# Kernel optimization log

Measured on AMD Instinct MI355X. Metric: run time of the kernel, lower is better.

The kernel has to match this reference:

```python
import jax, jax.numpy as jnp
import numpy as np

N_NODES = 50000
N_EDGES = 800000
IN_DIM = 100
OUT_DIM = 40
K_HOPS = 3


def setup_inputs() -> dict:
    key = jax.random.key(0)
    k1, k2, k3, k4 = jax.random.split(key, 4)
    feat = jax.random.normal(k1, (N_NODES, IN_DIM), dtype=jnp.float32)
    # fc params (PyTorch Linear default init scale ~ 1/sqrt(in_dim))
    W = jax.random.normal(k2, (OUT_DIM, IN_DIM), dtype=jnp.float32) / np.sqrt(IN_DIM)
    b = jnp.zeros((OUT_DIM,), dtype=jnp.float32)
    src = jax.random.randint(k3, (N_EDGES,), 0, N_NODES, dtype=jnp.int32)
    dst = jax.random.randint(k4, (N_EDGES,), 0, N_NODES, dtype=jnp.int32)
    return {"feat": feat, "W": W, "b": b, "src": src, "dst": dst}


def reference(feat, W, b, src, dst):
    n = feat.shape[0]
    # symmetric degree norm (DGL SGConv uses in-degrees, clamp(min=1))
    deg = jax.ops.segment_sum(jnp.ones_like(dst, dtype=feat.dtype), dst, num_segments=n)
    norm = jnp.maximum(deg, 1.0)[:, None] ** -0.5  # [N,1]
    h = feat
    for _ in range(K_HOPS):
        h = h * norm
        # SpMM: sum over incoming edges (gather src rows, scatter-add to dst)
        h = jax.ops.segment_sum(h[src], dst, num_segments=n)
        h = h * norm
    # user-supplied normalize: per-feature zero mean / unit std (unbiased std)
    h = (h - h.mean(axis=0)) / h.std(axis=0, ddof=1)
    # final linear classifier
    return h @ W.T + b
```

## Files before the change

kernel.cpp:

```cpp
#include <hip/hip_runtime.h>

#define N_NODES 50000
#define N_EDGES 800000
#define IN_DIM 100
#define OUT_DIM 40
#define ROW 50
#define ROW_PAD 64
#define SCAN_B 512
#define NSCAN_BLK ((N_NODES + SCAN_B - 1) / SCAN_B)
#define CSR_CAP (N_EDGES + N_NODES * 8 + 64)

typedef unsigned int uint;

__device__ __forceinline__ float bflo(uint u) { return __uint_as_float(u << 16); }
__device__ __forceinline__ float bfhi(uint u) { return __uint_as_float(u & 0xffff0000u); }
__device__ __forceinline__ uint packbf(float a, float b) {
    uint ua = __float_as_uint(a), ub = __float_as_uint(b);
    ua = (ua + 0x7fffu + ((ua >> 16) & 1u)) >> 16;
    ub = (ub + 0x7fffu + ((ub >> 16) & 1u)) >> 16;
    return ua | (ub << 16);
}

__global__ void zero_kernel(int* p, int n, uint* fs, uint* bufA, uint* bufB) {
    int i = blockIdx.x * blockDim.x + threadIdx.x;
    if (i < n) p[i] = 0;
    if (i < ROW_PAD) {
        fs[(size_t)N_NODES * ROW_PAD + i] = 0u;
        bufA[(size_t)N_NODES * ROW_PAD + i] = 0u;
        bufB[(size_t)N_NODES * ROW_PAD + i] = 0u;
    }
}

__global__ void deg_kernel(const int* __restrict__ dst, int* __restrict__ deg,
                           int* __restrict__ eoff) {
    int e = blockIdx.x * blockDim.x + threadIdx.x;
    if (e < N_EDGES) eoff[e] = atomicAdd(&deg[dst[e]], 1);
}

__global__ __launch_bounds__(SCAN_B) void scan1_kernel(const int* __restrict__ deg,
                                                       int* __restrict__ rowptr,
                                                       float* __restrict__ norm,
                                                       float* __restrict__ norm2,
                                                       int* __restrict__ blocksum) {
    int i = blockIdx.x * SCAN_B + threadIdx.x;
    int lane = threadIdx.x & 63, wid = threadIdx.x >> 6;
    int d = (i < N_NODES) ? deg[i] : 0;
    int da = (d + 7) & ~7;
    int v = da;
#pragma unroll
    for (int off = 1; off < 64; off <<= 1) {
        int t = __shfl_up(v, off);
        if (lane >= off) v += t;
    }
    __shared__ int wsum[8];
    if (lane == 63) wsum[wid] = v;
    __syncthreads();
    if (threadIdx.x < 8) {
        int w = wsum[threadIdx.x];
#pragma unroll
        for (int off = 1; off < 8; off <<= 1) {
            int t = __shfl_up(w, off);
            if (lane >= off) w += t;
        }
        wsum[threadIdx.x] = w;
    }
    __syncthreads();
    int woff = wid ? wsum[wid - 1] : 0;
    int incl = woff + v;
    if (i < N_NODES) {
        rowptr[i] = incl - da;
        float n1 = 1.0f / sqrtf((float)max(d, 1));
        norm[i] = n1;
        norm2[i] = n1 * n1;
    }
    if (threadIdx.x == SCAN_B - 1) blocksum[blockIdx.x] = incl;
}

__global__ __launch_bounds__(128) void scan2_kernel(const int* __restrict__ blocksum,
                                                    int* __restrict__ blockoff,
                                                    int* __restrict__ rowptr) {
    __shared__ int s[128];
    int t = threadIdx.x;
    int v = (t < NSCAN_BLK) ? blocksum[t] : 0;
    s[t] = v;
    __syncthreads();
    for (int off = 1; off < 128; off <<= 1) {
        int u = (t >= off) ? s[t - off] : 0;
        __syncthreads();
        s[t] += u;
        __syncthreads();
    }
    if (t < NSCAN_BLK) blockoff[t] = s[t] - v;
    if (t == 127) rowptr[N_NODES] = s[127];
}

__global__ __launch_bounds__(SCAN_B) void scan3_kernel(int* __restrict__ rowptr,
                                                       const int* __restrict__ blockoff,
                                                       const int* __restrict__ deg,
                                                       int* __restrict__ csr) {
    int i = blockIdx.x * SCAN_B + threadIdx.x;
    if (i < N_NODES) {
        int rp = rowptr[i] + blockoff[blockIdx.x];
        rowptr[i] = rp;
        int d = deg[i], da = (d + 7) & ~7;
        for (int k = d; k < da; ++k) csr[rp + k] = N_NODES;
    }
}

__global__ void csr_fill_kernel(const int* __restrict__ src, const int* __restrict__ dst,
                                const int* __restrict__ rowptr,
                                const int* __restrict__ eoff,
                                int* __restrict__ csr) {
    int e = blockIdx.x * blockDim.x + threadIdx.x;
    if (e < N_EDGES) csr[rowptr[dst[e]] + eoff[e]] = src[e];
}

__global__ __launch_bounds__(256) void prescale_kernel(const float* __restrict__ feat,
                                                       const float* __restrict__ norm,
                                                       uint4* __restrict__ fs4) {
    int t = blockIdx.x * 256 + threadIdx.x;
    if (t >= N_NODES * 16) return;
    int n = t >> 4, ql = t & 15;
    float nm = norm[n];
    uint4 o = make_uint4(0u, 0u, 0u, 0u);
    const float4* fr = (const float4*)(feat + (size_t)n * IN_DIM);
    if (ql < 12) {
        float4 a = fr[2 * ql], b2 = fr[2 * ql + 1];
        o.x = packbf(a.x * nm, a.y * nm);  o.y = packbf(a.z * nm, a.w * nm);
        o.z = packbf(b2.x * nm, b2.y * nm); o.w = packbf(b2.z * nm, b2.w * nm);
    } else if (ql == 12) {
        float4 a = fr[24];
        o.x = packbf(a.x * nm, a.y * nm);  o.y = packbf(a.z * nm, a.w * nm);
    }
    fs4[t] = o;
}

__global__ __launch_bounds__(128) void spmm_half_kernel(const uint4* __restrict__ H4,
                                                        const int* __restrict__ rowptr,
                                                        const int* __restrict__ csr,
                                                        const float* __restrict__ scale,
                                                        uint4* __restrict__ out4,
                                                        int off4) {
    const int n = blockIdx.x * 2 + (threadIdx.x >> 6);
    const int l = threadIdx.x & 63;
    const int e = l >> 3;
    const int ql = l & 7;
    const int beg = rowptr[n], end = rowptr[n + 1];
    float ax0 = 0.f, ax1 = 0.f, ax2 = 0.f, ax3 = 0.f;
    float ay0 = 0.f, ay1 = 0.f, ay2 = 0.f, ay3 = 0.f;
    for (int j = beg; j < end; j += 8) {
        int s = csr[j + e];
        uint4 u = H4[(size_t)s * 16 + off4 + ql];
        ax0 += bflo(u.x); ay0 += bfhi(u.x);
        ax1 += bflo(u.y); ay1 += bfhi(u.y);
        ax2 += bflo(u.z); ay2 += bfhi(u.z);
        ax3 += bflo(u.w); ay3 += bfhi(u.w);
    }
#pragma unroll
    for (int m = 8; m <= 32; m <<= 1) {
        ax0 += __shfl_xor(ax0, m); ax1 += __shfl_xor(ax1, m);
        ax2 += __shfl_xor(ax2, m); ax3 += __shfl_xor(ax3, m);
        ay0 += __shfl_xor(ay0, m); ay1 += __shfl_xor(ay1, m);
        ay2 += __shfl_xor(ay2, m); ay3 += __shfl_xor(ay3, m);
    }
    if (e == 0) {
        float sc = scale[n];
        uint4 o;
        o.x = packbf(ax0 * sc, ay0 * sc);
        o.y = packbf(ax1 * sc, ay1 * sc);
        o.z = packbf(ax2 * sc, ay2 * sc);
        o.w = packbf(ax3 * sc, ay3 * sc);
        out4[(size_t)n * 16 + off4 + ql] = o;
    }
}

#define CS_BLOCKS 625
#define CS_THREADS 256
__global__ __launch_bounds__(CS_THREADS) void col_stats_kernel(const uint* __restrict__ h,
                                                               float* __restrict__ colsum,
                                                               float* __restrict__ colsq) {
    int gtid = blockIdx.x * CS_THREADS + threadIdx.x;
    const int stride = CS_BLOCKS * CS_THREADS;
    const int total = N_NODES * ROW_PAD;
    float s0 = 0.f, s1 = 0.f, q0 = 0.f, q1 = 0.f;
    for (int i = gtid; i < total; i += stride) {
        uint u = h[i];
        float a = bflo(u), b = bfhi(u);
        s0 += a; s1 += b; q0 += a * a; q1 += b * b;
    }
    __shared__ float ssum[IN_DIM], ssq[IN_DIM];
    if (threadIdx.x < IN_DIM) { ssum[threadIdx.x] = 0.f; ssq[threadIdx.x] = 0.f; }
    __syncthreads();
    int p = gtid & 63;
    if (p < ROW) {
        atomicAdd(&ssum[2 * p], s0);
        atomicAdd(&ssum[2 * p + 1], s1);
        atomicAdd(&ssq[2 * p], q0);
        atomicAdd(&ssq[2 * p + 1], q1);
    }
    __syncthreads();
    if (threadIdx.x < IN_DIM) {
        atomicAdd(&colsum[threadIdx.x], ssum[threadIdx.x]);
        atomicAdd(&colsq[threadIdx.x], ssq[threadIdx.x]);
    }
}

__global__ __launch_bounds__(256) void prep_kernel(const float* __restrict__ colsum,
                                                   const float* __restrict__ colsq,
                                                   const float* __restrict__ W,
                                                   const float* __restrict__ b,
                                                   float* __restrict__ Wt,
                                                   float* __restrict__ bp) {
    __shared__ float smean[IN_DIM];
    __shared__ float sinv[IN_DIM];
    int t = threadIdx.x;
    const float Nf = (float)N_NODES;
    if (t < IN_DIM) {
        float m = colsum[t] / Nf;
        float var = (colsq[t] - Nf * m * m) / (Nf - 1.0f);
        var = fmaxf(var, 1e-20f);
        smean[t] = m;
        sinv[t] = 1.0f / sqrtf(var);
    }
    __syncthreads();
    for (int i = t; i < IN_DIM * OUT_DIM; i += 256) {
        int o = i % OUT_DIM, f = i / OUT_DIM;
        Wt[f * OUT_DIM + o] = W[o * IN_DIM + f] * sinv[f];
    }
    if (t < OUT_DIM) {
        float acc = b[t];
        for (int f = 0; f < IN_DIM; ++f)
            acc -= smean[f] * W[t * IN_DIM + f] * sinv[f];
        bp[t] = acc;
    }
}

__global__ __launch_bounds__(256) void final_kernel(const uint4* __restrict__ h4,
                                                    const float* __restrict__ Wt,
                                                    const float* __restrict__ bp,
                                                    float* __restrict__ out) {
    __shared__ float sW[104 * OUT_DIM];
    __shared__ float sb[OUT_DIM];
    for (int i = threadIdx.x; i < 104 * OUT_DIM; i += 256)
        sW[i] = (i < IN_DIM * OUT_DIM) ? Wt[i] : 0.f;
    if (threadIdx.x < OUT_DIM) sb[threadIdx.x] = bp[threadIdx.x];
    __syncthreads();
    int t = blockIdx.x * 256 + threadIdx.x;
    if (t >= N_NODES * 10) return;
    int n = t / 10;
    int og = (t - n * 10) * 4;
    const uint4* hr = h4 + (size_t)n * 16;
    float a0 = sb[og], a1 = sb[og + 1], a2 = sb[og + 2], a3 = sb[og + 3];
#pragma unroll
    for (int r = 0; r < 13; ++r) {
        uint4 u = hr[r];
        int f = r * 8;
        float v0 = bflo(u.x), v1 = bfhi(u.x), v2 = bflo(u.y), v3 = bfhi(u.y);
        float v4 = bflo(u.z), v5 = bfhi(u.z), v6 = bflo(u.w), v7 = bfhi(u.w);
        const float* w0 = &sW[(f + 0) * OUT_DIM + og];
        const float* w1 = &sW[(f + 1) * OUT_DIM + og];
        const float* w2 = &sW[(f + 2) * OUT_DIM + og];
        const float* w3 = &sW[(f + 3) * OUT_DIM + og];
        const float* w4 = &sW[(f + 4) * OUT_DIM + og];
        const float* w5 = &sW[(f + 5) * OUT_DIM + og];
        const float* w6 = &sW[(f + 6) * OUT_DIM + og];
        const float* w7 = &sW[(f + 7) * OUT_DIM + og];
        a0 += v0 * w0[0] + v1 * w1[0] + v2 * w2[0] + v3 * w3[0]
            + v4 * w4[0] + v5 * w5[0] + v6 * w6[0] + v7 * w7[0];
        a1 += v0 * w0[1] + v1 * w1[1] + v2 * w2[1] + v3 * w3[1]
            + v4 * w4[1] + v5 * w5[1] + v6 * w6[1] + v7 * w7[1];
        a2 += v0 * w0[2] + v1 * w1[2] + v2 * w2[2] + v3 * w3[2]
            + v4 * w4[2] + v5 * w5[2] + v6 * w6[2] + v7 * w7[2];
        a3 += v0 * w0[3] + v1 * w1[3] + v2 * w2[3] + v3 * w3[3]
            + v4 * w4[3] + v5 * w5[3] + v6 * w6[3] + v7 * w7[3];
    }
    float4 o = make_float4(a0, a1, a2, a3);
    *((float4*)(out + (size_t)n * OUT_DIM + og)) = o;
}

extern "C" void kernel_launch(void* const* d_in, const int* in_sizes, int n_in,
                              void* d_out, int out_size, void* d_ws, size_t ws_size,
                              hipStream_t stream) {
    const float* feat = (const float*)d_in[0];
    const float* W    = (const float*)d_in[1];
    const float* b    = (const float*)d_in[2];
    const int*   src  = (const int*)d_in[3];
    const int*   dst  = (const int*)d_in[4];
    float* out = (float*)d_out;

    char* w = (char*)d_ws;
    int*   deg      = (int*)w;    w += N_NODES * 4;
    float* colsum   = (float*)w;  w += 128 * 4;
    float* colsq    = (float*)w;  w += 128 * 4;
    int*   eoff     = (int*)w;    w += N_EDGES * 4;
    int*   rowptr   = (int*)w;    w += 50004 * 4;
    float* norm     = (float*)w;  w += N_NODES * 4;
    float* norm2    = (float*)w;  w += N_NODES * 4;
    int*   blocksum = (int*)w;    w += 128 * 4;
    int*   blockoff = (int*)w;    w += 128 * 4;
    int*   csr      = (int*)w;    w += CSR_CAP * 4;
    float* Wt       = (float*)w;  w += IN_DIM * OUT_DIM * 4;
    float* bp       = (float*)w;  w += 64 * 4;
    w = (char*)(((size_t)w + 255) & ~(size_t)255);
    const size_t HB = (size_t)(N_NODES + 1) * ROW_PAD * 4;
    uint*  fs       = (uint*)w;   w += HB;
    uint*  bufA     = (uint*)w;   w += HB;
    uint*  bufB     = (uint*)w;   w += HB;

    {
        int nz = N_NODES + 256;
        zero_kernel<<<(nz + 255) / 256, 256, 0, stream>>>(deg, nz, fs, bufA, bufB);
    }
    deg_kernel<<<(N_EDGES + 255) / 256, 256, 0, stream>>>(dst, deg, eoff);
    scan1_kernel<<<NSCAN_BLK, SCAN_B, 0, stream>>>(deg, rowptr, norm, norm2, blocksum);
    scan2_kernel<<<1, 128, 0, stream>>>(blocksum, blockoff, rowptr);
    scan3_kernel<<<NSCAN_BLK, SCAN_B, 0, stream>>>(rowptr, blockoff, deg, csr);
    csr_fill_kernel<<<(N_EDGES + 255) / 256, 256, 0, stream>>>(src, dst, rowptr, eoff, csr);
    prescale_kernel<<<(N_NODES * 16 + 255) / 256, 256, 0, stream>>>(feat, norm, (uint4*)fs);
    for (int off4 = 0; off4 <= 8; off4 += 8) {
        spmm_half_kernel<<<N_NODES / 2, 128, 0, stream>>>((const uint4*)fs,   rowptr, csr, norm2, (uint4*)bufA, off4);
        spmm_half_kernel<<<N_NODES / 2, 128, 0, stream>>>((const uint4*)bufA, rowptr, csr, norm2, (uint4*)bufB, off4);
        spmm_half_kernel<<<N_NODES / 2, 128, 0, stream>>>((const uint4*)bufB, rowptr, csr, norm,  (uint4*)bufA, off4);
    }
    col_stats_kernel<<<CS_BLOCKS, CS_THREADS, 0, stream>>>(bufA, colsum, colsq);
    prep_kernel<<<1, 256, 0, stream>>>(colsum, colsq, W, b, Wt, bp);
    {
        int total = N_NODES * 10;
        final_kernel<<<(total + 255) / 256, 256, 0, stream>>>((const uint4*)bufA, Wt, bp, out);
    }
}
```

Measured before the change: 318.2 us.

## Shard CSR by source half and split SpMM into two source-range passes

The CSR is rebuilt so each destination row holds two padded segments, one for sources in the lower half of the node range and one for the upper half. Each hop becomes two kernels: the first gathers from low-half sources into an fp32 accumulator, and the second gathers from high-half sources, adds the accumulator, scales, and writes bf16. Each pass now covers the full 64-uint row per node instead of running the hop twice over feature halves. The intent is to shrink the gather working set per pass so it stays cache-resident. The cost is extra accumulator traffic, more padding, and two nodes per wave with interleaved gathers.

```diff
diff --git a/kernel.cpp b/kernel.cpp
--- a/kernel.cpp
+++ b/kernel.cpp
@@ -8,9 +8,11 @@
 #define ROW_PAD 64
 #define SCAN_B 512
 #define NSCAN_BLK ((N_NODES + SCAN_B - 1) / SCAN_B)
-#define CSR_CAP (N_EDGES + N_NODES * 8 + 64)
+#define CSR_CAP (N_EDGES + N_NODES * 16 + 64)
+#define SHARD_SPLIT (N_NODES / 2)
 
 typedef unsigned int uint;
+typedef float f4 __attribute__((ext_vector_type(4)));
 
 __device__ __forceinline__ float bflo(uint u) { return __uint_as_float(u << 16); }
 __device__ __forceinline__ float bfhi(uint u) { return __uint_as_float(u & 0xffff0000u); }
@@ -31,21 +33,26 @@
     }
 }
 
-__global__ void deg_kernel(const int* __restrict__ dst, int* __restrict__ deg,
-                           int* __restrict__ eoff) {
+__global__ void deg_kernel(const int* __restrict__ src, const int* __restrict__ dst,
+                           int* __restrict__ deg2, int* __restrict__ eoff) {
     int e = blockIdx.x * blockDim.x + threadIdx.x;
-    if (e < N_EDGES) eoff[e] = atomicAdd(&deg[dst[e]], 1);
-}
-
-__global__ __launch_bounds__(SCAN_B) void scan1_kernel(const int* __restrict__ deg,
+    if (e < N_EDGES) {
+        int s = (src[e] >= SHARD_SPLIT) ? 1 : 0;
+        eoff[e] = atomicAdd(&deg2[2 * dst[e] + s], 1);
+    }
+}
+
+__global__ __launch_bounds__(SCAN_B) void scan1_kernel(const int* __restrict__ deg2,
                                                        int* __restrict__ rowptr,
                                                        float* __restrict__ norm,
                                                        float* __restrict__ norm2,
                                                        int* __restrict__ blocksum) {
     int i = blockIdx.x * SCAN_B + threadIdx.x;
     int lane = threadIdx.x & 63, wid = threadIdx.x >> 6;
-    int d = (i < N_NODES) ? deg[i] : 0;
-    int da = (d + 7) & ~7;
+    int d0 = (i < N_NODES) ? deg2[2 * i] : 0;
+    int d1 = (i < N_NODES) ? deg2[2 * i + 1] : 0;
+    int d = d0 + d1;
+    int da = ((d0 + 7) & ~7) + ((d1 + 7) & ~7);
     int v = da;
 #pragma unroll
     for (int off = 1; off < 64; off <<= 1) {
@@ -96,23 +103,32 @@
 
 __global__ __launch_bounds__(SCAN_B) void scan3_kernel(int* __restrict__ rowptr,
                                                        const int* __restrict__ blockoff,
-                                                       const int* __restrict__ deg,
+                                                       const int* __restrict__ deg2,
                                                        int* __restrict__ csr) {
     int i = blockIdx.x * SCAN_B + threadIdx.x;
     if (i < N_NODES) {
         int rp = rowptr[i] + blockoff[blockIdx.x];
         rowptr[i] = rp;
-        int d = deg[i], da = (d + 7) & ~7;
-        for (int k = d; k < da; ++k) csr[rp + k] = N_NODES;
+        int d0 = deg2[2 * i], d1 = deg2[2 * i + 1];
+        int da0 = (d0 + 7) & ~7, da1 = (d1 + 7) & ~7;
+        for (int k = d0; k < da0; ++k) csr[rp + k] = N_NODES;
+        for (int k = d1; k < da1; ++k) csr[rp + da0 + k] = N_NODES;
     }
 }
 
 __global__ void csr_fill_kernel(const int* __restrict__ src, const int* __restrict__ dst,
                                 const int* __restrict__ rowptr,
+                                const int* __restrict__ deg2,
                                 const int* __restrict__ eoff,
                                 int* __restrict__ csr) {
     int e = blockIdx.x * blockDim.x + threadIdx.x;
-    if (e < N_EDGES) csr[rowptr[dst[e]] + eoff[e]] = src[e];
+    if (e < N_EDGES) {
+        int d = dst[e];
+        int sv = src[e];
+        int base = rowptr[d];
+        if (sv >= SHARD_SPLIT) base += (deg2[2 * d] + 7) & ~7;
+        csr[base + eoff[e]] = sv;
+    }
 }
 
 __global__ __launch_bounds__(256) void prescale_kernel(const float* __restrict__ feat,
@@ -135,42 +151,130 @@
     fs4[t] = o;
 }
 
-__global__ __launch_bounds__(128) void spmm_half_kernel(const uint4* __restrict__ H4,
-                                                        const int* __restrict__ rowptr,
-                                                        const int* __restrict__ csr,
-                                                        const float* __restrict__ scale,
-                                                        uint4* __restrict__ out4,
-                                                        int off4) {
-    const int n = blockIdx.x * 2 + (threadIdx.x >> 6);
+
+#define GATHER2(jj, ee, sX, sY)                                            \
+    int sX = (jj < ee) ? csr[jj + q] : (int)N_NODES;                       \
+    int sY = (jj < ee) ? csr[jj + 4 + q] : (int)N_NODES;
+
+#define ACC8(u, x0, y0, x1, y1, x2, y2, x3, y3)                            \
+    x0 += bflo(u.x); y0 += bfhi(u.x);                                      \
+    x1 += bflo(u.y); y1 += bfhi(u.y);                                      \
+    x2 += bflo(u.z); y2 += bfhi(u.z);                                      \
+    x3 += bflo(u.w); y3 += bfhi(u.w);
+
+#define RED8(x0, y0, x1, y1, x2, y2, x3, y3, m)                            \
+    x0 += __shfl_xor(x0, m); y0 += __shfl_xor(y0, m);                      \
+    x1 += __shfl_xor(x1, m); y1 += __shfl_xor(y1, m);                      \
+    x2 += __shfl_xor(x2, m); y2 += __shfl_xor(y2, m);                      \
+    x3 += __shfl_xor(x3, m); y3 += __shfl_xor(y3, m);
+
+__global__ __launch_bounds__(128) void spmmA_kernel(const uint4* __restrict__ H4,
+                                                    const int* __restrict__ rowptr,
+                                                    const int* __restrict__ deg2,
+                                                    const int* __restrict__ csr,
+                                                    float* __restrict__ accum) {
+    const int wave = threadIdx.x >> 6;
+    const int n0 = (blockIdx.x * 2 + wave) * 2;
+    const int n1 = n0 + 1;
     const int l = threadIdx.x & 63;
-    const int e = l >> 3;
-    const int ql = l & 7;
-    const int beg = rowptr[n], end = rowptr[n + 1];
-    float ax0 = 0.f, ax1 = 0.f, ax2 = 0.f, ax3 = 0.f;
-    float ay0 = 0.f, ay1 = 0.f, ay2 = 0.f, ay3 = 0.f;
-    for (int j = beg; j < end; j += 8) {
-        int s = csr[j + e];
-        uint4 u = H4[(size_t)s * 16 + off4 + ql];
-        ax0 += bflo(u.x); ay0 += bfhi(u.x);
-        ax1 += bflo(u.y); ay1 += bfhi(u.y);
-        ax2 += bflo(u.z); ay2 += bfhi(u.z);
-        ax3 += bflo(u.w); ay3 += bfhi(u.w);
-    }
-#pragma unroll
-    for (int m = 8; m <= 32; m <<= 1) {
-        ax0 += __shfl_xor(ax0, m); ax1 += __shfl_xor(ax1, m);
-        ax2 += __shfl_xor(ax2, m); ax3 += __shfl_xor(ax3, m);
-        ay0 += __shfl_xor(ay0, m); ay1 += __shfl_xor(ay1, m);
-        ay2 += __shfl_xor(ay2, m); ay3 += __shfl_xor(ay3, m);
-    }
-    if (e == 0) {
-        float sc = scale[n];
+    const int q = l >> 4, ql = l & 15;
+    int j0 = rowptr[n0], e0 = j0 + ((deg2[2 * n0] + 7) & ~7);
+    int j1 = rowptr[n1], e1 = j1 + ((deg2[2 * n1] + 7) & ~7);
+    float ax0 = 0.f, ay0 = 0.f, ax1 = 0.f, ay1 = 0.f,
+          ax2 = 0.f, ay2 = 0.f, ax3 = 0.f, ay3 = 0.f;
+    float bx0 = 0.f, by0 = 0.f, bx1 = 0.f, by1 = 0.f,
+          bx2 = 0.f, by2 = 0.f, bx3 = 0.f, by3 = 0.f;
+    while (j0 < e0 || j1 < e1) {
+        GATHER2(j0, e0, sA0, sA1)
+        GATHER2(j1, e1, sB0, sB1)
+        uint4 u0 = H4[(size_t)sA0 * 16 + ql];
+        uint4 u1 = H4[(size_t)sA1 * 16 + ql];
+        uint4 u2 = H4[(size_t)sB0 * 16 + ql];
+        uint4 u3 = H4[(size_t)sB1 * 16 + ql];
+        ACC8(u0, ax0, ay0, ax1, ay1, ax2, ay2, ax3, ay3)
+        ACC8(u1, ax0, ay0, ax1, ay1, ax2, ay2, ax3, ay3)
+        ACC8(u2, bx0, by0, bx1, by1, bx2, by2, bx3, by3)
+        ACC8(u3, bx0, by0, bx1, by1, bx2, by2, bx3, by3)
+        j0 += 8; j1 += 8;
+    }
+    RED8(ax0, ay0, ax1, ay1, ax2, ay2, ax3, ay3, 16)
+    RED8(ax0, ay0, ax1, ay1, ax2, ay2, ax3, ay3, 32)
+    RED8(bx0, by0, bx1, by1, bx2, by2, bx3, by3, 16)
+    RED8(bx0, by0, bx1, by1, bx2, by2, bx3, by3, 32)
+    if (q == 0) {
+        float* p = accum + (size_t)n0 * 128 + ql * 8;
+        f4 v0 = {ax0, ay0, ax1, ay1};
+        f4 v1 = {ax2, ay2, ax3, ay3};
+        __builtin_nontemporal_store(v0, (f4*)p);
+        __builtin_nontemporal_store(v1, (f4*)(p + 4));
+    } else if (q == 1) {
+        float* p = accum + (size_t)n1 * 128 + ql * 8;
+        f4 v0 = {bx0, by0, bx1, by1};
+        f4 v1 = {bx2, by2, bx3, by3};
+        __builtin_nontemporal_store(v0, (f4*)p);
+        __builtin_nontemporal_store(v1, (f4*)(p + 4));
+    }
+}
+
+__global__ __launch_bounds__(128) void spmmB_kernel(const uint4* __restrict__ H4,
+                                                    const int* __restrict__ rowptr,
+                                                    const int* __restrict__ deg2,
+                                                    const int* __restrict__ csr,
+                                                    const float* __restrict__ accum,
+                                                    const float* __restrict__ scale,
+                                                    uint4* __restrict__ out4) {
+    const int wave = threadIdx.x >> 6;
+    const int n0 = (blockIdx.x * 2 + wave) * 2;
+    const int n1 = n0 + 1;
+    const int l = threadIdx.x & 63;
+    const int q = l >> 4, ql = l & 15;
+    int rp0 = rowptr[n0], rp1 = rowptr[n1];
+    int da00 = (deg2[2 * n0] + 7) & ~7, da10 = (deg2[2 * n1] + 7) & ~7;
+    int j0 = rp0 + da00, e0 = j0 + ((deg2[2 * n0 + 1] + 7) & ~7);
+    int j1 = rp1 + da10, e1 = j1 + ((deg2[2 * n1 + 1] + 7) & ~7);
+    float ax0 = 0.f, ay0 = 0.f, ax1 = 0.f, ay1 = 0.f,
+          ax2 = 0.f, ay2 = 0.f, ax3 = 0.f, ay3 = 0.f;
+    float bx0 = 0.f, by0 = 0.f, bx1 = 0.f, by1 = 0.f,
+          bx2 = 0.f, by2 = 0.f, bx3 = 0.f, by3 = 0.f;
+    while (j0 < e0 || j1 < e1) {
+        GATHER2(j0, e0, sA0, sA1)
+        GATHER2(j1, e1, sB0, sB1)
+        uint4 u0 = H4[(size_t)sA0 * 16 + ql];
+        uint4 u1 = H4[(size_t)sA1 * 16 + ql];
+        uint4 u2 = H4[(size_t)sB0 * 16 + ql];
+        uint4 u3 = H4[(size_t)sB1 * 16 + ql];
+        ACC8(u0, ax0, ay0, ax1, ay1, ax2, ay2, ax3, ay3)
+        ACC8(u1, ax0, ay0, ax1, ay1, ax2, ay2, ax3, ay3)
+        ACC8(u2, bx0, by0, bx1, by1, bx2, by2, bx3, by3)
+        ACC8(u3, bx0, by0, bx1, by1, bx2, by2, bx3, by3)
+        j0 += 8; j1 += 8;
+    }
+    RED8(ax0, ay0, ax1, ay1, ax2, ay2, ax3, ay3, 16)
+    RED8(ax0, ay0, ax1, ay1, ax2, ay2, ax3, ay3, 32)
+    RED8(bx0, by0, bx1, by1, bx2, by2, bx3, by3, 16)
+    RED8(bx0, by0, bx1, by1, bx2, by2, bx3, by3, 32)
+    if (q == 0) {
+        const float* p = accum + (size_t)n0 * 128 + ql * 8;
+        f4 w0 = __builtin_nontemporal_load((const f4*)p);
+        f4 w1 = __builtin_nontemporal_load((const f4*)(p + 4));
+        float sc = scale[n0];
         uint4 o;
-        o.x = packbf(ax0 * sc, ay0 * sc);
-        o.y = packbf(ax1 * sc, ay1 * sc);
-        o.z = packbf(ax2 * sc, ay2 * sc);
-        o.w = packbf(ax3 * sc, ay3 * sc);
-        out4[(size_t)n * 16 + off4 + ql] = o;
+        o.x = packbf((ax0 + w0.x) * sc, (ay0 + w0.y) * sc);
+        o.y = packbf((ax1 + w0.z) * sc, (ay1 + w0.w) * sc);
+        o.z = packbf((ax2 + w1.x) * sc, (ay2 + w1.y) * sc);
+        o.w = packbf((ax3 + w1.z) * sc, (ay3 + w1.w) * sc);
+        out4[(size_t)n0 * 16 + ql] = o;
+    } else if (q == 1) {
+        const float* p = accum + (size_t)n1 * 128 + ql * 8;
+        f4 w0 = __builtin_nontemporal_load((const f4*)p);
+        f4 w1 = __builtin_nontemporal_load((const f4*)(p + 4));
+        float sc = scale[n1];
+        uint4 o;
+        o.x = packbf((bx0 + w0.x) * sc, (by0 + w0.y) * sc);
+        o.y = packbf((bx1 + w0.z) * sc, (by1 + w0.w) * sc);
+        o.z = packbf((bx2 + w1.x) * sc, (by2 + w1.y) * sc);
+        o.w = packbf((bx3 + w1.z) * sc, (by3 + w1.w) * sc);
+        out4[(size_t)n1 * 16 + ql] = o;
     }
 }
 
@@ -289,7 +393,7 @@
     float* out = (float*)d_out;
 
     char* w = (char*)d_ws;
-    int*   deg      = (int*)w;    w += N_NODES * 4;
+    int*   deg2     = (int*)w;    w += 2 * N_NODES * 4;
     float* colsum   = (float*)w;  w += 128 * 4;
     float* colsq    = (float*)w;  w += 128 * 4;
     int*   eoff     = (int*)w;    w += N_EDGES * 4;
@@ -306,21 +410,26 @@
     uint*  fs       = (uint*)w;   w += HB;
     uint*  bufA     = (uint*)w;   w += HB;
     uint*  bufB     = (uint*)w;   w += HB;
+    float* accum    = (float*)w;  w += (size_t)N_NODES * 128 * 4;
 
     {
-        int nz = N_NODES + 256;
-        zero_kernel<<<(nz + 255) / 256, 256, 0, stream>>>(deg, nz, fs, bufA, bufB);
-    }
-    deg_kernel<<<(N_EDGES + 255) / 256, 256, 0, stream>>>(dst, deg, eoff);
-    scan1_kernel<<<NSCAN_BLK, SCAN_B, 0, stream>>>(deg, rowptr, norm, norm2, blocksum);
+        int nz = 2 * N_NODES + 256;
+        zero_kernel<<<(nz + 255) / 256, 256, 0, stream>>>(deg2, nz, fs, bufA, bufB);
+    }
+    deg_kernel<<<(N_EDGES + 255) / 256, 256, 0, stream>>>(src, dst, deg2, eoff);
+    scan1_kernel<<<NSCAN_BLK, SCAN_B, 0, stream>>>(deg2, rowptr, norm, norm2, blocksum);
     scan2_kernel<<<1, 128, 0, stream>>>(blocksum, blockoff, rowptr);
-    scan3_kernel<<<NSCAN_BLK, SCAN_B, 0, stream>>>(rowptr, blockoff, deg, csr);
-    csr_fill_kernel<<<(N_EDGES + 255) / 256, 256, 0, stream>>>(src, dst, rowptr, eoff, csr);
+    scan3_kernel<<<NSCAN_BLK, SCAN_B, 0, stream>>>(rowptr, blockoff, deg2, csr);
+    csr_fill_kernel<<<(N_EDGES + 255) / 256, 256, 0, stream>>>(src, dst, rowptr, deg2, eoff, csr);
     prescale_kernel<<<(N_NODES * 16 + 255) / 256, 256, 0, stream>>>(feat, norm, (uint4*)fs);
-    for (int off4 = 0; off4 <= 8; off4 += 8) {
-        spmm_half_kernel<<<N_NODES / 2, 128, 0, stream>>>((const uint4*)fs,   rowptr, csr, norm2, (uint4*)bufA, off4);
-        spmm_half_kernel<<<N_NODES / 2, 128, 0, stream>>>((const uint4*)bufA, rowptr, csr, norm2, (uint4*)bufB, off4);
-        spmm_half_kernel<<<N_NODES / 2, 128, 0, stream>>>((const uint4*)bufB, rowptr, csr, norm,  (uint4*)bufA, off4);
+    {
+        const int G = N_NODES / 4;
+        spmmA_kernel<<<G, 128, 0, stream>>>((const uint4*)fs, rowptr, deg2, csr, accum);
+        spmmB_kernel<<<G, 128, 0, stream>>>((const uint4*)fs, rowptr, deg2, csr, accum, norm2, (uint4*)bufA);
+        spmmA_kernel<<<G, 128, 0, stream>>>((const uint4*)bufA, rowptr, deg2, csr, accum);
+        spmmB_kernel<<<G, 128, 0, stream>>>((const uint4*)bufA, rowptr, deg2, csr, accum, norm2, (uint4*)bufB);
+        spmmA_kernel<<<G, 128, 0, stream>>>((const uint4*)bufB, rowptr, deg2, csr, accum);
+        spmmB_kernel<<<G, 128, 0, stream>>>((const uint4*)bufB, rowptr, deg2, csr, accum, norm, (uint4*)bufA);
     }
     col_stats_kernel<<<CS_BLOCKS, CS_THREADS, 0, stream>>>(bufA, colsum, colsq);
     prep_kernel<<<1, 256, 0, stream>>>(colsum, colsq, W, b, Wt, bp);
```

New measurement: 319.7 us. Within noise of the previous version (+0.5%).
